# Kernel tuning notes

Measured on AMD Instinct MI355X. Metric: run time of the kernel, lower is better.

## Reference

```python
import jax, jax.numpy as jnp
import numpy as np

N_OSC = 2  # n: oscillator group size (pairwise oscillators)


def group_norm(c, w, b, num_groups, eps=1e-5):
    # c: [B, C, N]; torch.nn.GroupNorm semantics over (group-channels, N)
    B, C, N = c.shape
    g = c.reshape(B, num_groups, C // num_groups, N)
    mu = g.mean(axis=(2, 3), keepdims=True)
    var = g.var(axis=(2, 3), keepdims=True)
    g = (g - mu) / jnp.sqrt(var + eps)
    return g.reshape(B, C, N) * w[None, :, None] + b[None, :, None]


def normalize(x, n=N_OSC, eps=1e-6):
    # project each size-n group of channels onto the unit sphere
    B, N, C = x.shape
    v = x.reshape(B, N, C // n, n)
    nrm = jnp.linalg.norm(v, axis=-1, keepdims=True)
    return (v / (nrm + eps)).reshape(B, N, C)


def setup_inputs():
    key = jax.random.key(0)
    ks = jax.random.split(key, 4)
    B, C, N = 2, 16, 8192
    x = jax.random.normal(ks[0], (B, C, N), jnp.float32)
    c = jax.random.normal(ks[1], (B, C, N), jnp.float32)
    sc = jax.random.uniform(ks[2], (1, N, N), jnp.float32)  # dense structural connectivity
    gn_w = jnp.ones((C,), jnp.float32)
    gn_b = jnp.zeros((C,), jnp.float32)
    # learned per-edge coupling weight; scaled ~1/N so coupling is O(1)
    conn_w = jax.random.normal(ks[3], (N, N), jnp.float32) * (1.0 / N)
    # OmegaLayer param: init_omg * (1/sqrt(2)) * ones((ch//2, 1))
    omg_param = jnp.full((C // 2, 1), 1.0 / np.sqrt(2), jnp.float32)
    gamma = jnp.ones((1,), jnp.float32)
    return {"x": x, "c": c, "sc": sc, "gn_w": gn_w, "gn_b": gn_b,
            "conn_w": conn_w, "omg_param": omg_param, "gamma": gamma, "Q": 8}


def reference(x, c, sc, gn_w, gn_b, conn_w, omg_param, gamma, Q):
    n = N_OSC
    C = x.shape[1]
    # c_norm (GroupNorm with ch//n groups) then transpose [B,C,N] -> [B,N,C]
    y = group_norm(c, gn_w, gn_b, C // n)
    y = jnp.swapaxes(y, 1, 2)  # [B,N,C]
    xt = jnp.swapaxes(x, 1, 2)  # [B,N,C]
    A = sc[0] * conn_w  # weighted adjacency [N,N]
    omg = jnp.abs(omg_param)[None, None, :, 0]  # [1,1,C//2]; norm over last dim == abs
    g = gamma.reshape(())
    xt = normalize(xt)
    B, N, _ = xt.shape

    def step(xk, _):
        coup = jnp.einsum('mn,bnc->bmc', A, xk)  # graph coupling
        yt = coup + y
        xv = xk.reshape(B, N, C // n, n)
        yv = yt.reshape(B, N, C // n, n)
        sim = jnp.sum(xv * yv, axis=-1, keepdims=True)  # <x, y> per group
        y_proj = (yv - sim * xv).reshape(B, N, C)  # tangent projection
        xp = xk.reshape(B, N, C // 2, 2)
        omg_x = jnp.stack([omg * xp[..., 1], -omg * xp[..., 0]], axis=-1).reshape(B, N, C)
        xn = normalize(xk + g * (omg_x + y_proj))
        return xn, xn

    _, xs = jax.lax.scan(step, xt, None, length=Q)
    return xs  # [Q, B, N, C] (stacked list of per-step states)
```

## Files before the change

kernel.cpp:

```cpp
#include <hip/hip_runtime.h>
#include <hip/hip_bf16.h>

#define NB 2
#define NC 16
#define NN 8192
#define NBC 32
#define KS 16
#define SROWS 16
#define SWAVES 8
#define KCH 512
#define NCHUNK (NN / KCH)
#define ROWPITCH 520
#define STEP_ELEMS (NB * NN * NC)

typedef float f32x4 __attribute__((ext_vector_type(4)));
typedef __bf16 bf16x8 __attribute__((ext_vector_type(8)));

__global__ void gn_stats_k(const float* __restrict__ c, float* __restrict__ stats) {
    int bg = blockIdx.x;
    const float* p = c + (size_t)bg * 16384;
    float s = 0.f, ss = 0.f;
    for (int i = threadIdx.x; i < 4096; i += 256) {
        float4 v = ((const float4*)p)[i];
        s  += v.x + v.y + v.z + v.w;
        ss += v.x*v.x + v.y*v.y + v.z*v.z + v.w*v.w;
    }
    #pragma unroll
    for (int o = 32; o; o >>= 1) { s += __shfl_down(s, o); ss += __shfl_down(ss, o); }
    __shared__ float sh[8];
    int w = threadIdx.x >> 6;
    if ((threadIdx.x & 63) == 0) { sh[w] = s; sh[w + 4] = ss; }
    __syncthreads();
    if (threadIdx.x == 0) {
        float S = sh[0]+sh[1]+sh[2]+sh[3], SS = sh[4]+sh[5]+sh[6]+sh[7];
        float mu = S * (1.f/16384.f);
        float var = SS * (1.f/16384.f) - mu*mu;
        stats[bg*2]   = mu;
        stats[bg*2+1] = rsqrtf(var + 1e-5f);
    }
}

__global__ void prep_xy_k(const float* __restrict__ x, const float* __restrict__ c,
                          const float* __restrict__ gnw, const float* __restrict__ gnb,
                          const float* __restrict__ stats,
                          float* __restrict__ y_arr, float* __restrict__ x0f,
                          __bf16* __restrict__ Xbf) {
    int tid = blockIdx.x * 256 + threadIdx.x;
    int n = tid & (NN - 1);
    int j = (tid >> 13) & 7;
    int b = tid >> 16;
    int ch0 = 2 * j;
    size_t r0 = ((size_t)(b * NC + ch0)) * NN + n;
    float c0 = c[r0], c1 = c[r0 + NN];
    float x0 = x[r0], x1 = x[r0 + NN];
    float mu = stats[(b*8 + j)*2], rstd = stats[(b*8 + j)*2 + 1];
    float y0 = (c0 - mu) * rstd * gnw[ch0]   + gnb[ch0];
    float y1 = (c1 - mu) * rstd * gnw[ch0+1] + gnb[ch0+1];
    int base = n * NBC + b * NC + ch0;
    y_arr[base] = y0; y_arr[base + 1] = y1;
    float inv = 1.f / (sqrtf(x0*x0 + x1*x1) + 1e-6f);
    x0 *= inv; x1 *= inv;
    size_t xi = ((size_t)(b * NN + n)) * NC + ch0;
    x0f[xi] = x0; x0f[xi + 1] = x1;
    Xbf[(size_t)(b*NC + ch0)     * NN + n] = (__bf16)x0;
    Xbf[(size_t)(b*NC + ch0 + 1) * NN + n] = (__bf16)x1;
}

__global__ void prep_A_k(const float* __restrict__ sc, const float* __restrict__ cw,
                         __bf16* __restrict__ Abf) {
    size_t i = ((size_t)blockIdx.x * 256 + threadIdx.x) * 8;
    f32x4 s0 = ((const f32x4*)(sc + i))[0], s1 = ((const f32x4*)(sc + i))[1];
    f32x4 w0 = ((const f32x4*)(cw + i))[0], w1 = ((const f32x4*)(cw + i))[1];
    bf16x8 o;
    o[0]=(__bf16)(s0[0]*w0[0]); o[1]=(__bf16)(s0[1]*w0[1]);
    o[2]=(__bf16)(s0[2]*w0[2]); o[3]=(__bf16)(s0[3]*w0[3]);
    o[4]=(__bf16)(s1[0]*w1[0]); o[5]=(__bf16)(s1[1]*w1[1]);
    o[6]=(__bf16)(s1[2]*w1[2]); o[7]=(__bf16)(s1[3]*w1[3]);
    *(bf16x8*)(Abf + i) = o;
}

__global__ __launch_bounds__(512, 4) void gemm_stage_k(
    const __bf16* __restrict__ Abf, const __bf16* __restrict__ Xc,
    float* __restrict__ coup)
{
    __shared__ __align__(16) __bf16 Abuf[2][SROWS * ROWPITCH];
    __shared__ float red[SWAVES][SROWS][36];
    int tid = threadIdx.x;
    int lane = tid & 63, w = tid >> 6;
    int mb = blockIdx.x;

    int r0 = 2 * w;
    const __bf16* asrc0 = Abf + (size_t)(mb * SROWS + r0) * NN + lane * 8;
    const __bf16* asrc1 = asrc0 + NN;

    int fr = lane & 15;
    int kg = (lane >> 4) * 8;
    const __bf16* xb0 = Xc + (size_t)fr * NN + w * 64 + kg;
    const __bf16* xb1 = xb0 + (size_t)16 * NN;
    const __bf16* ab  = &Abuf[0][fr * ROWPITCH + w * 64 + kg];
    const int abstride = SROWS * ROWPITCH;

    f32x4 acc0 = {0.f,0.f,0.f,0.f}, acc1 = {0.f,0.f,0.f,0.f};

    __builtin_amdgcn_global_load_lds(
        (const __attribute__((address_space(1))) void*)(asrc0),
        (__attribute__((address_space(3))) void*)(&Abuf[0][r0 * ROWPITCH]), 16, 0, 0);
    __builtin_amdgcn_global_load_lds(
        (const __attribute__((address_space(1))) void*)(asrc1),
        (__attribute__((address_space(3))) void*)(&Abuf[0][(r0 + 1) * ROWPITCH]), 16, 0, 0);
    __syncthreads();

    int buf = 0;
    for (int c = 0; c < NCHUNK; ++c) {
        bf16x8 b00 = *(const bf16x8*)(xb0 + c * KCH);
        bf16x8 b01 = *(const bf16x8*)(xb0 + c * KCH + 32);
        bf16x8 b10 = *(const bf16x8*)(xb1 + c * KCH);
        bf16x8 b11 = *(const bf16x8*)(xb1 + c * KCH + 32);
        if (c + 1 < NCHUNK) {
            int nb = buf ^ 1;
            __builtin_amdgcn_global_load_lds(
                (const __attribute__((address_space(1))) void*)(asrc0 + (c + 1) * KCH),
                (__attribute__((address_space(3))) void*)(&Abuf[nb][r0 * ROWPITCH]), 16, 0, 0);
            __builtin_amdgcn_global_load_lds(
                (const __attribute__((address_space(1))) void*)(asrc1 + (c + 1) * KCH),
                (__attribute__((address_space(3))) void*)(&Abuf[nb][(r0 + 1) * ROWPITCH]), 16, 0, 0);
        }
        const __bf16* ac = ab + buf * abstride;
        bf16x8 a0 = *(const bf16x8*)(ac);
        bf16x8 a1 = *(const bf16x8*)(ac + 32);
        acc0 = __builtin_amdgcn_mfma_f32_16x16x32_bf16(a0, b00, acc0, 0, 0, 0);
        acc1 = __builtin_amdgcn_mfma_f32_16x16x32_bf16(a0, b10, acc1, 0, 0, 0);
        acc0 = __builtin_amdgcn_mfma_f32_16x16x32_bf16(a1, b01, acc0, 0, 0, 0);
        acc1 = __builtin_amdgcn_mfma_f32_16x16x32_bf16(a1, b11, acc1, 0, 0, 0);
        __syncthreads();
        buf ^= 1;
    }

    int orow = (lane >> 4) * 4, ocol = lane & 15;
    #pragma unroll
    for (int r4 = 0; r4 < 4; ++r4) {
        red[w][orow + r4][ocol]      = acc0[r4];
        red[w][orow + r4][ocol + 16] = acc1[r4];
    }
    __syncthreads();

    if (tid < SROWS * 16) {
        int ch2 = tid & 15;
        int r_  = tid >> 4;
        float c0 = 0.f, c1 = 0.f;
        #pragma unroll
        for (int ww = 0; ww < SWAVES; ++ww) {
            c0 += red[ww][r_][2 * ch2];
            c1 += red[ww][r_][2 * ch2 + 1];
        }
        int n_ = mb * SROWS + r_;
        coup[(size_t)n_ * NBC + 2 * ch2]     = c0;
        coup[(size_t)n_ * NBC + 2 * ch2 + 1] = c1;
    }
}

__global__ void update_coup_k(const float* __restrict__ coup, const float* __restrict__ y_arr,
                              const float* __restrict__ omg, const float* __restrict__ gamma,
                              float* __restrict__ x0f, __bf16* __restrict__ Xbf,
                              float* __restrict__ out_k) {
    int tid = blockIdx.x * 256 + threadIdx.x;
    int pi = tid & 15;
    int b = pi >> 3, j = pi & 7;
    int n = tid >> 4;
    int base = n * NBC + b * NC + 2 * j;
    float c0 = coup[base];
    float c1 = coup[base + 1];
    float y0 = y_arr[base] + c0;
    float y1 = y_arr[base + 1] + c1;
    size_t xi = ((size_t)(b * NN + n)) * NC + 2 * j;
    float x0 = x0f[xi], x1 = x0f[xi + 1];
    float sim = x0 * y0 + x1 * y1;
    float p0 = y0 - sim * x0;
    float p1 = y1 - sim * x1;
    float om = fabsf(omg[j]);
    float g  = gamma[0];
    float v0 = x0 + g * ( om * x1 + p0);
    float v1 = x1 + g * (-om * x0 + p1);
    float inv = 1.f / (sqrtf(v0*v0 + v1*v1) + 1e-6f);
    v0 *= inv; v1 *= inv;
    out_k[xi] = v0; out_k[xi + 1] = v1;
    x0f[xi] = v0; x0f[xi + 1] = v1;
    Xbf[(size_t)(b*NC + 2*j)     * NN + n] = (__bf16)v0;
    Xbf[(size_t)(b*NC + 2*j + 1) * NN + n] = (__bf16)v1;
}

__device__ inline bf16x8 mulcvt8(const float* __restrict__ s, const float* __restrict__ w) {
    f32x4 s0 = ((const f32x4*)s)[0], s1 = ((const f32x4*)s)[1];
    f32x4 w0 = ((const f32x4*)w)[0], w1 = ((const f32x4*)w)[1];
    bf16x8 r;
    r[0]=(__bf16)(s0[0]*w0[0]); r[1]=(__bf16)(s0[1]*w0[1]);
    r[2]=(__bf16)(s0[2]*w0[2]); r[3]=(__bf16)(s0[3]*w0[3]);
    r[4]=(__bf16)(s1[0]*w1[0]); r[5]=(__bf16)(s1[1]*w1[1]);
    r[6]=(__bf16)(s1[2]*w1[2]); r[7]=(__bf16)(s1[3]*w1[3]);
    return r;
}

__global__ __launch_bounds__(256) void gemm_step_fused_k(const float* __restrict__ sc,
                                                         const float* __restrict__ cw,
                                                         const __bf16* __restrict__ Xbf,
                                                         float* __restrict__ part) {
    int mb = blockIdx.x;
    int ks = blockIdx.y;
    int lane = threadIdx.x & 63;
    int w = threadIdx.x >> 6;
    int row = mb * 64 + w * 16 + (lane & 15);
    int kb  = (lane >> 4) * 8;
    int k0  = ks * (NN / KS);
    const int KC = NN / KS;
    f32x4 acc0 = {0.f,0.f,0.f,0.f}, acc1 = {0.f,0.f,0.f,0.f};
    const __bf16* bp0 = Xbf + (size_t)(lane & 15) * NN + k0 + kb;
    const __bf16* bp1 = bp0 + (size_t)16 * NN;
    const float* as = sc + (size_t)row * NN + k0 + kb;
    const float* aw = cw + (size_t)row * NN + k0 + kb;
    #pragma unroll 4
    for (int k = 0; k < KC; k += 32) {
        bf16x8 a  = mulcvt8(as + k, aw + k);
        bf16x8 b0 = *(const bf16x8*)(bp0 + k);
        bf16x8 b1 = *(const bf16x8*)(bp1 + k);
        acc0 = __builtin_amdgcn_mfma_f32_16x16x32_bf16(a, b0, acc0, 0, 0, 0);
        acc1 = __builtin_amdgcn_mfma_f32_16x16x32_bf16(a, b1, acc1, 0, 0, 0);
    }
    int orow = mb * 64 + w * 16 + (lane >> 4) * 4;
    int ocol = lane & 15;
    float* pp = part + (size_t)ks * NN * NBC + (size_t)orow * NBC + ocol;
    #pragma unroll
    for (int r = 0; r < 4; ++r) {
        pp[(size_t)r * NBC]      = acc0[r];
        pp[(size_t)r * NBC + 16] = acc1[r];
    }
}

__global__ void update_step_k(const float* __restrict__ part, const float* __restrict__ y_arr,
                              const float* __restrict__ omg, const float* __restrict__ gamma,
                              float* __restrict__ x0f, __bf16* __restrict__ Xbf,
                              float* __restrict__ out_k) {
    int tid = blockIdx.x * 256 + threadIdx.x;
    int pi = tid & 15;
    int b = pi >> 3, j = pi & 7;
    int n = tid >> 4;
    int base = n * NBC + b * NC + 2 * j;
    float c0 = 0.f, c1 = 0.f;
    #pragma unroll
    for (int ks = 0; ks < KS; ++ks) {
        const float* p = part + (size_t)ks * NN * NBC + base;
        c0 += p[0]; c1 += p[1];
    }
    float y0 = y_arr[base] + c0;
    float y1 = y_arr[base + 1] + c1;
    size_t xi = ((size_t)(b * NN + n)) * NC + 2 * j;
    float x0 = x0f[xi], x1 = x0f[xi + 1];
    float sim = x0 * y0 + x1 * y1;
    float p0 = y0 - sim * x0;
    float p1 = y1 - sim * x1;
    float om = fabsf(omg[j]);
    float g  = gamma[0];
    float v0 = x0 + g * ( om * x1 + p0);
    float v1 = x1 + g * (-om * x0 + p1);
    float inv = 1.f / (sqrtf(v0*v0 + v1*v1) + 1e-6f);
    v0 *= inv; v1 *= inv;
    out_k[xi] = v0; out_k[xi + 1] = v1;
    x0f[xi] = v0; x0f[xi + 1] = v1;
    Xbf[(size_t)(b*NC + 2*j)     * NN + n] = (__bf16)v0;
    Xbf[(size_t)(b*NC + 2*j + 1) * NN + n] = (__bf16)v1;
}

extern "C" void kernel_launch(void* const* d_in, const int* in_sizes, int n_in,
                              void* d_out, int out_size, void* d_ws, size_t ws_size,
                              hipStream_t stream) {
    const float* x     = (const float*)d_in[0];
    const float* c     = (const float*)d_in[1];
    const float* sc    = (const float*)d_in[2];
    const float* gnw   = (const float*)d_in[3];
    const float* gnb   = (const float*)d_in[4];
    const float* cw    = (const float*)d_in[5];
    const float* omg   = (const float*)d_in[6];
    const float* gamma = (const float*)d_in[7];
    float* out = (float*)d_out;
    int Q = out_size / STEP_ELEMS;

    const size_t szA    = (size_t)NN * NN * 2;
    const size_t szX    = (size_t)NBC * NN * 2;
    const size_t szX0f  = (size_t)NB * NN * NC * 4;
    const size_t szY    = (size_t)NN * NBC * 4;
    const size_t szCoup = (size_t)NN * NBC * 4;
    const size_t szPart = (size_t)KS * NN * NBC * 4;
    const size_t rest = szX + szX0f + szY + szCoup + szPart + 256;
    bool bigws = ws_size >= szA + rest;

    char* p = (char*)d_ws;
    __bf16* Abf = nullptr;
    if (bigws) { Abf = (__bf16*)p; p += szA; }
    __bf16* Xbf  = (__bf16*)p; p += szX;
    float* x0f   = (float*)p;  p += szX0f;
    float* y_arr = (float*)p;  p += szY;
    float* coup  = (float*)p;  p += szCoup;
    float* part  = (float*)p;  p += szPart;
    float* stats = (float*)p;  p += 256;

    gn_stats_k<<<16, 256, 0, stream>>>(c, stats);
    prep_xy_k<<<(NB * NN * 8) / 256, 256, 0, stream>>>(x, c, gnw, gnb, stats, y_arr, x0f, Xbf);

    if (bigws) {
        prep_A_k<<<((size_t)NN * NN / 8) / 256, 256, 0, stream>>>(sc, cw, Abf);
        for (int q = 0; q < Q; ++q) {
            gemm_stage_k<<<NN / SROWS, SWAVES * 64, 0, stream>>>(Abf, Xbf, coup);
            update_coup_k<<<(NB * NN * 8) / 256, 256, 0, stream>>>(
                coup, y_arr, omg, gamma, x0f, Xbf, out + (size_t)q * STEP_ELEMS);
        }
    } else {
        dim3 gg(NN / 64, KS);
        for (int q = 0; q < Q; ++q) {
            gemm_step_fused_k<<<gg, 256, 0, stream>>>(sc, cw, Xbf, part);
            update_step_k<<<(NB * NN * 8) / 256, 256, 0, stream>>>(
                part, y_arr, omg, gamma, x0f, Xbf, out + (size_t)q * STEP_ELEMS);
        }
    }
}
```

Baseline: 491.2 us.

## Fuse adjacency conversion into first GEMM step and double K-chunk size

Removes the separate prep_A pass: the first step's GEMM kernel now reads sc and conn_w in fp32, multiplies and converts them to bf16, stages the result in LDS for its own MFMA work, and writes the bf16 adjacency to the workspace for later steps. This avoids re-reading the bf16 matrix right after writing it. The later-step GEMM kernel now processes 1024-wide K chunks with four MFMA pairs per chunk and reuses the same shared buffer for the reduction scratch. The larger LDS footprint may limit how many blocks fit per CU, and the fused first step uses register loads instead of direct global-to-LDS copies.

```diff
diff --git a/kernel.cpp b/kernel.cpp
--- a/kernel.cpp
+++ b/kernel.cpp
@@ -8,10 +8,15 @@
 #define KS 16
 #define SROWS 16
 #define SWAVES 8
+#define STEP_ELEMS (NB * NN * NC)
+
 #define KCH 512
 #define NCHUNK (NN / KCH)
 #define ROWPITCH 520
-#define STEP_ELEMS (NB * NN * NC)
+
+#define KCH2 1024
+#define NCHUNK2 (NN / KCH2)
+#define ROWPITCH2 1032
 
 typedef float f32x4 __attribute__((ext_vector_type(4)));
 typedef __bf16 bf16x8 __attribute__((ext_vector_type(8)));
@@ -66,21 +71,18 @@
     Xbf[(size_t)(b*NC + ch0 + 1) * NN + n] = (__bf16)x1;
 }
 
-__global__ void prep_A_k(const float* __restrict__ sc, const float* __restrict__ cw,
-                         __bf16* __restrict__ Abf) {
-    size_t i = ((size_t)blockIdx.x * 256 + threadIdx.x) * 8;
-    f32x4 s0 = ((const f32x4*)(sc + i))[0], s1 = ((const f32x4*)(sc + i))[1];
-    f32x4 w0 = ((const f32x4*)(cw + i))[0], w1 = ((const f32x4*)(cw + i))[1];
-    bf16x8 o;
-    o[0]=(__bf16)(s0[0]*w0[0]); o[1]=(__bf16)(s0[1]*w0[1]);
-    o[2]=(__bf16)(s0[2]*w0[2]); o[3]=(__bf16)(s0[3]*w0[3]);
-    o[4]=(__bf16)(s1[0]*w1[0]); o[5]=(__bf16)(s1[1]*w1[1]);
-    o[6]=(__bf16)(s1[2]*w1[2]); o[7]=(__bf16)(s1[3]*w1[3]);
-    *(bf16x8*)(Abf + i) = o;
-}
-
-__global__ __launch_bounds__(512, 4) void gemm_stage_k(
-    const __bf16* __restrict__ Abf, const __bf16* __restrict__ Xc,
+__device__ inline bf16x8 cvt8(f32x4 s0, f32x4 s1, f32x4 w0, f32x4 w1) {
+    bf16x8 r;
+    r[0]=(__bf16)(s0[0]*w0[0]); r[1]=(__bf16)(s0[1]*w0[1]);
+    r[2]=(__bf16)(s0[2]*w0[2]); r[3]=(__bf16)(s0[3]*w0[3]);
+    r[4]=(__bf16)(s1[0]*w1[0]); r[5]=(__bf16)(s1[1]*w1[1]);
+    r[6]=(__bf16)(s1[2]*w1[2]); r[7]=(__bf16)(s1[3]*w1[3]);
+    return r;
+}
+
+__global__ __launch_bounds__(512, 4) void gemm_conv_k(
+    const float* __restrict__ sc, const float* __restrict__ cw,
+    __bf16* __restrict__ Abf, const __bf16* __restrict__ Xc,
     float* __restrict__ coup)
 {
     __shared__ __align__(16) __bf16 Abuf[2][SROWS * ROWPITCH];
@@ -90,8 +92,9 @@
     int mb = blockIdx.x;
 
     int r0 = 2 * w;
-    const __bf16* asrc0 = Abf + (size_t)(mb * SROWS + r0) * NN + lane * 8;
-    const __bf16* asrc1 = asrc0 + NN;
+    size_t rowbase0 = (size_t)(mb * SROWS + r0) * NN;
+    size_t rowbase1 = rowbase0 + NN;
+    int le = lane * 8;
 
     int fr = lane & 15;
     int kg = (lane >> 4) * 8;
@@ -102,12 +105,18 @@
 
     f32x4 acc0 = {0.f,0.f,0.f,0.f}, acc1 = {0.f,0.f,0.f,0.f};
 
-    __builtin_amdgcn_global_load_lds(
-        (const __attribute__((address_space(1))) void*)(asrc0),
-        (__attribute__((address_space(3))) void*)(&Abuf[0][r0 * ROWPITCH]), 16, 0, 0);
-    __builtin_amdgcn_global_load_lds(
-        (const __attribute__((address_space(1))) void*)(asrc1),
-        (__attribute__((address_space(3))) void*)(&Abuf[0][(r0 + 1) * ROWPITCH]), 16, 0, 0);
+    {
+        const f32x4* sp0 = (const f32x4*)(sc + rowbase0 + le);
+        const f32x4* wp0 = (const f32x4*)(cw + rowbase0 + le);
+        const f32x4* sp1 = (const f32x4*)(sc + rowbase1 + le);
+        const f32x4* wp1 = (const f32x4*)(cw + rowbase1 + le);
+        bf16x8 o0 = cvt8(sp0[0], sp0[1], wp0[0], wp0[1]);
+        bf16x8 o1 = cvt8(sp1[0], sp1[1], wp1[0], wp1[1]);
+        *(bf16x8*)(&Abuf[0][r0 * ROWPITCH + le])       = o0;
+        *(bf16x8*)(&Abuf[0][(r0 + 1) * ROWPITCH + le]) = o1;
+        *(bf16x8*)(Abf + rowbase0 + le) = o0;
+        *(bf16x8*)(Abf + rowbase1 + le) = o1;
+    }
     __syncthreads();
 
     int buf = 0;
@@ -116,14 +125,14 @@
         bf16x8 b01 = *(const bf16x8*)(xb0 + c * KCH + 32);
         bf16x8 b10 = *(const bf16x8*)(xb1 + c * KCH);
         bf16x8 b11 = *(const bf16x8*)(xb1 + c * KCH + 32);
+        f32x4 s0, s1, w0, w1, s2, s3, w2, w3;
         if (c + 1 < NCHUNK) {
-            int nb = buf ^ 1;
-            __builtin_amdgcn_global_load_lds(
-                (const __attribute__((address_space(1))) void*)(asrc0 + (c + 1) * KCH),
-                (__attribute__((address_space(3))) void*)(&Abuf[nb][r0 * ROWPITCH]), 16, 0, 0);
-            __builtin_amdgcn_global_load_lds(
-                (const __attribute__((address_space(1))) void*)(asrc1 + (c + 1) * KCH),
-                (__attribute__((address_space(3))) void*)(&Abuf[nb][(r0 + 1) * ROWPITCH]), 16, 0, 0);
+            size_t o0 = rowbase0 + (size_t)(c + 1) * KCH + le;
+            size_t o1 = rowbase1 + (size_t)(c + 1) * KCH + le;
+            s0 = ((const f32x4*)(sc + o0))[0]; s1 = ((const f32x4*)(sc + o0))[1];
+            w0 = ((const f32x4*)(cw + o0))[0]; w1 = ((const f32x4*)(cw + o0))[1];
+            s2 = ((const f32x4*)(sc + o1))[0]; s3 = ((const f32x4*)(sc + o1))[1];
+            w2 = ((const f32x4*)(cw + o1))[0]; w3 = ((const f32x4*)(cw + o1))[1];
         }
         const __bf16* ac = ab + buf * abstride;
         bf16x8 a0 = *(const bf16x8*)(ac);
@@ -132,6 +141,104 @@
         acc1 = __builtin_amdgcn_mfma_f32_16x16x32_bf16(a0, b10, acc1, 0, 0, 0);
         acc0 = __builtin_amdgcn_mfma_f32_16x16x32_bf16(a1, b01, acc0, 0, 0, 0);
         acc1 = __builtin_amdgcn_mfma_f32_16x16x32_bf16(a1, b11, acc1, 0, 0, 0);
+        if (c + 1 < NCHUNK) {
+            int nb = buf ^ 1;
+            bf16x8 o0 = cvt8(s0, s1, w0, w1);
+            bf16x8 o1 = cvt8(s2, s3, w2, w3);
+            *(bf16x8*)(&Abuf[nb][r0 * ROWPITCH + le])       = o0;
+            *(bf16x8*)(&Abuf[nb][(r0 + 1) * ROWPITCH + le]) = o1;
+            *(bf16x8*)(Abf + rowbase0 + (size_t)(c + 1) * KCH + le) = o0;
+            *(bf16x8*)(Abf + rowbase1 + (size_t)(c + 1) * KCH + le) = o1;
+        }
+        __syncthreads();
+        buf ^= 1;
+    }
+
+    int orow = (lane >> 4) * 4, ocol = lane & 15;
+    #pragma unroll
+    for (int r4 = 0; r4 < 4; ++r4) {
+        red[w][orow + r4][ocol]      = acc0[r4];
+        red[w][orow + r4][ocol + 16] = acc1[r4];
+    }
+    __syncthreads();
+
+    if (tid < SROWS * 16) {
+        int ch2 = tid & 15;
+        int r_  = tid >> 4;
+        float c0 = 0.f, c1 = 0.f;
+        #pragma unroll
+        for (int ww = 0; ww < SWAVES; ++ww) {
+            c0 += red[ww][r_][2 * ch2];
+            c1 += red[ww][r_][2 * ch2 + 1];
+        }
+        int n_ = mb * SROWS + r_;
+        coup[(size_t)n_ * NBC + 2 * ch2]     = c0;
+        coup[(size_t)n_ * NBC + 2 * ch2 + 1] = c1;
+    }
+}
+
+__global__ __launch_bounds__(512, 4) void gemm_stage_k(
+    const __bf16* __restrict__ Abf, const __bf16* __restrict__ Xc,
+    float* __restrict__ coup)
+{
+    __shared__ __align__(16) char smem[2 * SROWS * ROWPITCH2 * 2];
+    __bf16 (*Abuf)[SROWS * ROWPITCH2] = (__bf16 (*)[SROWS * ROWPITCH2])smem;
+    float (*red)[SROWS][36] = (float (*)[SROWS][36])smem;
+    int tid = threadIdx.x;
+    int lane = tid & 63, w = tid >> 6;
+    int mb = blockIdx.x;
+
+    int r0 = 2 * w;
+    const __bf16* asrc0 = Abf + (size_t)(mb * SROWS + r0) * NN + lane * 8;
+    const __bf16* asrc1 = asrc0 + NN;
+
+    int fr = lane & 15;
+    int kg = (lane >> 4) * 8;
+    const __bf16* xb0 = Xc + (size_t)fr * NN + w * 128 + kg;
+    const __bf16* xb1 = xb0 + (size_t)16 * NN;
+    const __bf16* ab  = &Abuf[0][fr * ROWPITCH2 + w * 128 + kg];
+    const int abstride = SROWS * ROWPITCH2;
+
+    f32x4 acc0 = {0.f,0.f,0.f,0.f}, acc1 = {0.f,0.f,0.f,0.f};
+
+    #pragma unroll
+    for (int h = 0; h < 2; ++h) {
+        __builtin_amdgcn_global_load_lds(
+            (const __attribute__((address_space(1))) void*)(asrc0 + h * 512),
+            (__attribute__((address_space(3))) void*)(&Abuf[0][r0 * ROWPITCH2 + h * 512]), 16, 0, 0);
+        __builtin_amdgcn_global_load_lds(
+            (const __attribute__((address_space(1))) void*)(asrc1 + h * 512),
+            (__attribute__((address_space(3))) void*)(&Abuf[0][(r0 + 1) * ROWPITCH2 + h * 512]), 16, 0, 0);
+    }
+    __syncthreads();
+
+    int buf = 0;
+    for (int c = 0; c < NCHUNK2; ++c) {
+        bf16x8 bx0[4], bx1[4];
+        #pragma unroll
+        for (int s = 0; s < 4; ++s) {
+            bx0[s] = *(const bf16x8*)(xb0 + c * KCH2 + s * 32);
+            bx1[s] = *(const bf16x8*)(xb1 + c * KCH2 + s * 32);
+        }
+        if (c + 1 < NCHUNK2) {
+            int nb = buf ^ 1;
+            #pragma unroll
+            for (int h = 0; h < 2; ++h) {
+                __builtin_amdgcn_global_load_lds(
+                    (const __attribute__((address_space(1))) void*)(asrc0 + (size_t)(c + 1) * KCH2 + h * 512),
+                    (__attribute__((address_space(3))) void*)(&Abuf[nb][r0 * ROWPITCH2 + h * 512]), 16, 0, 0);
+                __builtin_amdgcn_global_load_lds(
+                    (const __attribute__((address_space(1))) void*)(asrc1 + (size_t)(c + 1) * KCH2 + h * 512),
+                    (__attribute__((address_space(3))) void*)(&Abuf[nb][(r0 + 1) * ROWPITCH2 + h * 512]), 16, 0, 0);
+            }
+        }
+        const __bf16* ac = ab + buf * abstride;
+        #pragma unroll
+        for (int s = 0; s < 4; ++s) {
+            bf16x8 a = *(const bf16x8*)(ac + s * 32);
+            acc0 = __builtin_amdgcn_mfma_f32_16x16x32_bf16(a, bx0[s], acc0, 0, 0, 0);
+            acc1 = __builtin_amdgcn_mfma_f32_16x16x32_bf16(a, bx1[s], acc1, 0, 0, 0);
+        }
         __syncthreads();
         buf ^= 1;
     }
@@ -192,12 +299,7 @@
 __device__ inline bf16x8 mulcvt8(const float* __restrict__ s, const float* __restrict__ w) {
     f32x4 s0 = ((const f32x4*)s)[0], s1 = ((const f32x4*)s)[1];
     f32x4 w0 = ((const f32x4*)w)[0], w1 = ((const f32x4*)w)[1];
-    bf16x8 r;
-    r[0]=(__bf16)(s0[0]*w0[0]); r[1]=(__bf16)(s0[1]*w0[1]);
-    r[2]=(__bf16)(s0[2]*w0[2]); r[3]=(__bf16)(s0[3]*w0[3]);
-    r[4]=(__bf16)(s1[0]*w1[0]); r[5]=(__bf16)(s1[1]*w1[1]);
-    r[6]=(__bf16)(s1[2]*w1[2]); r[7]=(__bf16)(s1[3]*w1[3]);
-    return r;
+    return cvt8(s0, s1, w0, w1);
 }
 
 __global__ __launch_bounds__(256) void gemm_step_fused_k(const float* __restrict__ sc,
@@ -306,9 +408,11 @@
     prep_xy_k<<<(NB * NN * 8) / 256, 256, 0, stream>>>(x, c, gnw, gnb, stats, y_arr, x0f, Xbf);
 
     if (bigws) {
-        prep_A_k<<<((size_t)NN * NN / 8) / 256, 256, 0, stream>>>(sc, cw, Abf);
         for (int q = 0; q < Q; ++q) {
-            gemm_stage_k<<<NN / SROWS, SWAVES * 64, 0, stream>>>(Abf, Xbf, coup);
+            if (q == 0)
+                gemm_conv_k<<<NN / SROWS, SWAVES * 64, 0, stream>>>(sc, cw, Abf, Xbf, coup);
+            else
+                gemm_stage_k<<<NN / SROWS, SWAVES * 64, 0, stream>>>(Abf, Xbf, coup);
             update_coup_k<<<(NB * NN * 8) / 256, 256, 0, stream>>>(
                 coup, y_arr, omg, gamma, x0f, Xbf, out + (size_t)q * STEP_ELEMS);
         }
```

Result: slower. 511.7 us (+4.2%).

## Pre-swizzle bf16 adjacency into MFMA fragment order and drop LDS staging

Applied to the files above, without the earlier changes.

The one-time prep kernel now writes the bf16 adjacency already permuted into the per-lane MFMA A-fragment layout, staging it through shared memory so the stores stay coalesced. Each wave can then load its A fragments straight from global memory with contiguous 16-byte loads. This removes the LDS double buffer and the per-chunk __syncthreads. The GEMM loop is now register-prefetched and fully unrolled, and each wave covers a contiguous 1024-wide K slice instead of interleaved 64-wide pieces. The cost is a more complex prep kernel and reliance on the global-load prefetch alone to hide latency.

```diff
diff --git a/kernel.cpp b/kernel.cpp
--- a/kernel.cpp
+++ b/kernel.cpp
@@ -8,9 +8,6 @@
 #define KS 16
 #define SROWS 16
 #define SWAVES 8
-#define KCH 512
-#define NCHUNK (NN / KCH)
-#define ROWPITCH 520
 #define STEP_ELEMS (NB * NN * NC)
 
 typedef float f32x4 __attribute__((ext_vector_type(4)));
@@ -66,75 +63,88 @@
     Xbf[(size_t)(b*NC + ch0 + 1) * NN + n] = (__bf16)x1;
 }
 
-__global__ void prep_A_k(const float* __restrict__ sc, const float* __restrict__ cw,
-                         __bf16* __restrict__ Abf) {
-    size_t i = ((size_t)blockIdx.x * 256 + threadIdx.x) * 8;
-    f32x4 s0 = ((const f32x4*)(sc + i))[0], s1 = ((const f32x4*)(sc + i))[1];
-    f32x4 w0 = ((const f32x4*)(cw + i))[0], w1 = ((const f32x4*)(cw + i))[1];
-    bf16x8 o;
-    o[0]=(__bf16)(s0[0]*w0[0]); o[1]=(__bf16)(s0[1]*w0[1]);
-    o[2]=(__bf16)(s0[2]*w0[2]); o[3]=(__bf16)(s0[3]*w0[3]);
-    o[4]=(__bf16)(s1[0]*w1[0]); o[5]=(__bf16)(s1[1]*w1[1]);
-    o[6]=(__bf16)(s1[2]*w1[2]); o[7]=(__bf16)(s1[3]*w1[3]);
-    *(bf16x8*)(Abf + i) = o;
-}
-
-__global__ __launch_bounds__(512, 4) void gemm_stage_k(
-    const __bf16* __restrict__ Abf, const __bf16* __restrict__ Xc,
+__device__ inline bf16x8 cvt8(f32x4 s0, f32x4 s1, f32x4 w0, f32x4 w1) {
+    bf16x8 r;
+    r[0]=(__bf16)(s0[0]*w0[0]); r[1]=(__bf16)(s0[1]*w0[1]);
+    r[2]=(__bf16)(s0[2]*w0[2]); r[3]=(__bf16)(s0[3]*w0[3]);
+    r[4]=(__bf16)(s1[0]*w1[0]); r[5]=(__bf16)(s1[1]*w1[1]);
+    r[6]=(__bf16)(s1[2]*w1[2]); r[7]=(__bf16)(s1[3]*w1[3]);
+    return r;
+}
+
+__global__ __launch_bounds__(256) void prep_A_frag_k(const float* __restrict__ sc,
+                                                     const float* __restrict__ cw,
+                                                     __bf16* __restrict__ Af) {
+    __shared__ __align__(16) __bf16 tb[16][520];
+    int t = threadIdx.x;
+    int p  = blockIdx.x >> 4;
+    int kc = blockIdx.x & 15;
+    #pragma unroll
+    for (int it = 0; it < 4; ++it) {
+        int e = it * 2048 + t * 8;
+        int row = e >> 9;
+        int kloc = e & 511;
+        size_t src = (size_t)(p * 16 + row) * NN + kc * 512 + kloc;
+        f32x4 s0 = ((const f32x4*)(sc + src))[0], s1 = ((const f32x4*)(sc + src))[1];
+        f32x4 w0 = ((const f32x4*)(cw + src))[0], w1 = ((const f32x4*)(cw + src))[1];
+        bf16x8 o = cvt8(s0, s1, w0, w1);
+        int k32 = kloc >> 5;
+        int lane_f = row + (((kloc & 31) >> 3) << 4);
+        *(bf16x8*)(&tb[k32][lane_f * 8]) = o;
+    }
+    __syncthreads();
+    size_t obase = ((size_t)p * 256 + kc * 16) * 512;
+    #pragma unroll
+    for (int it = 0; it < 4; ++it) {
+        int f = it * 256 + t;
+        int k32 = f >> 6;
+        int lf  = f & 63;
+        bf16x8 v = *(const bf16x8*)(&tb[k32][lf * 8]);
+        *(bf16x8*)(Af + obase + (size_t)f * 8) = v;
+    }
+}
+
+__global__ __launch_bounds__(512, 4) void gemm_frag_k(
+    const __bf16* __restrict__ Af, const __bf16* __restrict__ Xc,
     float* __restrict__ coup)
 {
-    __shared__ __align__(16) __bf16 Abuf[2][SROWS * ROWPITCH];
     __shared__ float red[SWAVES][SROWS][36];
     int tid = threadIdx.x;
     int lane = tid & 63, w = tid >> 6;
     int mb = blockIdx.x;
 
-    int r0 = 2 * w;
-    const __bf16* asrc0 = Abf + (size_t)(mb * SROWS + r0) * NN + lane * 8;
-    const __bf16* asrc1 = asrc0 + NN;
-
+    const __bf16* ap = Af + ((size_t)mb * 256 + w * 32) * 512 + lane * 8;
     int fr = lane & 15;
     int kg = (lane >> 4) * 8;
-    const __bf16* xb0 = Xc + (size_t)fr * NN + w * 64 + kg;
+    const __bf16* xb0 = Xc + (size_t)fr * NN + w * 1024 + kg;
     const __bf16* xb1 = xb0 + (size_t)16 * NN;
-    const __bf16* ab  = &Abuf[0][fr * ROWPITCH + w * 64 + kg];
-    const int abstride = SROWS * ROWPITCH;
 
     f32x4 acc0 = {0.f,0.f,0.f,0.f}, acc1 = {0.f,0.f,0.f,0.f};
 
-    __builtin_amdgcn_global_load_lds(
-        (const __attribute__((address_space(1))) void*)(asrc0),
-        (__attribute__((address_space(3))) void*)(&Abuf[0][r0 * ROWPITCH]), 16, 0, 0);
-    __builtin_amdgcn_global_load_lds(
-        (const __attribute__((address_space(1))) void*)(asrc1),
-        (__attribute__((address_space(3))) void*)(&Abuf[0][(r0 + 1) * ROWPITCH]), 16, 0, 0);
-    __syncthreads();
-
-    int buf = 0;
-    for (int c = 0; c < NCHUNK; ++c) {
-        bf16x8 b00 = *(const bf16x8*)(xb0 + c * KCH);
-        bf16x8 b01 = *(const bf16x8*)(xb0 + c * KCH + 32);
-        bf16x8 b10 = *(const bf16x8*)(xb1 + c * KCH);
-        bf16x8 b11 = *(const bf16x8*)(xb1 + c * KCH + 32);
-        if (c + 1 < NCHUNK) {
-            int nb = buf ^ 1;
-            __builtin_amdgcn_global_load_lds(
-                (const __attribute__((address_space(1))) void*)(asrc0 + (c + 1) * KCH),
-                (__attribute__((address_space(3))) void*)(&Abuf[nb][r0 * ROWPITCH]), 16, 0, 0);
-            __builtin_amdgcn_global_load_lds(
-                (const __attribute__((address_space(1))) void*)(asrc1 + (c + 1) * KCH),
-                (__attribute__((address_space(3))) void*)(&Abuf[nb][(r0 + 1) * ROWPITCH]), 16, 0, 0);
-        }
-        const __bf16* ac = ab + buf * abstride;
-        bf16x8 a0 = *(const bf16x8*)(ac);
-        bf16x8 a1 = *(const bf16x8*)(ac + 32);
+    bf16x8 a0  = *(const bf16x8*)(ap);
+    bf16x8 a1  = *(const bf16x8*)(ap + 512);
+    bf16x8 b00 = *(const bf16x8*)(xb0);
+    bf16x8 b01 = *(const bf16x8*)(xb0 + 32);
+    bf16x8 b10 = *(const bf16x8*)(xb1);
+    bf16x8 b11 = *(const bf16x8*)(xb1 + 32);
+    #pragma unroll
+    for (int it = 0; it < 15; ++it) {
+        bf16x8 na0  = *(const bf16x8*)(ap  + (2 * it + 2) * 512);
+        bf16x8 na1  = *(const bf16x8*)(ap  + (2 * it + 3) * 512);
+        bf16x8 nb00 = *(const bf16x8*)(xb0 + it * 64 + 64);
+        bf16x8 nb01 = *(const bf16x8*)(xb0 + it * 64 + 96);
+        bf16x8 nb10 = *(const bf16x8*)(xb1 + it * 64 + 64);
+        bf16x8 nb11 = *(const bf16x8*)(xb1 + it * 64 + 96);
         acc0 = __builtin_amdgcn_mfma_f32_16x16x32_bf16(a0, b00, acc0, 0, 0, 0);
         acc1 = __builtin_amdgcn_mfma_f32_16x16x32_bf16(a0, b10, acc1, 0, 0, 0);
         acc0 = __builtin_amdgcn_mfma_f32_16x16x32_bf16(a1, b01, acc0, 0, 0, 0);
         acc1 = __builtin_amdgcn_mfma_f32_16x16x32_bf16(a1, b11, acc1, 0, 0, 0);
-        __syncthreads();
-        buf ^= 1;
-    }
+        a0 = na0; a1 = na1; b00 = nb00; b01 = nb01; b10 = nb10; b11 = nb11;
+    }
+    acc0 = __builtin_amdgcn_mfma_f32_16x16x32_bf16(a0, b00, acc0, 0, 0, 0);
+    acc1 = __builtin_amdgcn_mfma_f32_16x16x32_bf16(a0, b10, acc1, 0, 0, 0);
+    acc0 = __builtin_amdgcn_mfma_f32_16x16x32_bf16(a1, b01, acc0, 0, 0, 0);
+    acc1 = __builtin_amdgcn_mfma_f32_16x16x32_bf16(a1, b11, acc1, 0, 0, 0);
 
     int orow = (lane >> 4) * 4, ocol = lane & 15;
     #pragma unroll
@@ -192,12 +202,7 @@
 __device__ inline bf16x8 mulcvt8(const float* __restrict__ s, const float* __restrict__ w) {
     f32x4 s0 = ((const f32x4*)s)[0], s1 = ((const f32x4*)s)[1];
     f32x4 w0 = ((const f32x4*)w)[0], w1 = ((const f32x4*)w)[1];
-    bf16x8 r;
-    r[0]=(__bf16)(s0[0]*w0[0]); r[1]=(__bf16)(s0[1]*w0[1]);
-    r[2]=(__bf16)(s0[2]*w0[2]); r[3]=(__bf16)(s0[3]*w0[3]);
-    r[4]=(__bf16)(s1[0]*w1[0]); r[5]=(__bf16)(s1[1]*w1[1]);
-    r[6]=(__bf16)(s1[2]*w1[2]); r[7]=(__bf16)(s1[3]*w1[3]);
-    return r;
+    return cvt8(s0, s1, w0, w1);
 }
 
 __global__ __launch_bounds__(256) void gemm_step_fused_k(const float* __restrict__ sc,
@@ -293,8 +298,8 @@
     bool bigws = ws_size >= szA + rest;
 
     char* p = (char*)d_ws;
-    __bf16* Abf = nullptr;
-    if (bigws) { Abf = (__bf16*)p; p += szA; }
+    __bf16* Af = nullptr;
+    if (bigws) { Af = (__bf16*)p; p += szA; }
     __bf16* Xbf  = (__bf16*)p; p += szX;
     float* x0f   = (float*)p;  p += szX0f;
     float* y_arr = (float*)p;  p += szY;
@@ -306,9 +311,9 @@
     prep_xy_k<<<(NB * NN * 8) / 256, 256, 0, stream>>>(x, c, gnw, gnb, stats, y_arr, x0f, Xbf);
 
     if (bigws) {
-        prep_A_k<<<((size_t)NN * NN / 8) / 256, 256, 0, stream>>>(sc, cw, Abf);
+        prep_A_frag_k<<<(NN / 16) * (NN / 512), 256, 0, stream>>>(sc, cw, Af);
         for (int q = 0; q < Q; ++q) {
-            gemm_stage_k<<<NN / SROWS, SWAVES * 64, 0, stream>>>(Abf, Xbf, coup);
+            gemm_frag_k<<<NN / SROWS, SWAVES * 64, 0, stream>>>(Af, Xbf, coup);
             update_coup_k<<<(NB * NN * 8) / 256, 256, 0, stream>>>(
                 coup, y_arr, omg, gamma, x0f, Xbf, out + (size_t)q * STEP_ELEMS);
         }
```

Measured after the change: 459.8 us. 6.4% less time.
